# Kernel tuning notes

Measured on AMD Instinct MI355X. Metric: run time of the kernel, lower is better.

The kernel has to match this reference:

```python
import jax, jax.numpy as jnp
import numpy as np

B, S, D, H = 2, 2048, 2048, 16
HD = D // H          # 128
HALF = HD // 2       # 64
EPS = 1e-6


def setup_inputs() -> dict:
    key = jax.random.key(0)
    ks = jax.random.split(key, 10)
    x = jax.random.normal(ks[0], (B, S, D), jnp.float32)
    # RoPE frequencies: standard theta=10000, per (position, half head dim)
    inv_freq = 1.0 / (10000.0 ** (np.arange(HALF, dtype=np.float64) / HALF))
    ang = np.outer(np.arange(S, dtype=np.float64), inv_freq)  # (S, HALF)
    freqs_cos = jnp.asarray(np.cos(ang), jnp.float32)[:, None, :]  # (S,1,HALF)
    freqs_sin = jnp.asarray(np.sin(ang), jnp.float32)[:, None, :]
    sc = 0.02
    qw = jax.random.normal(ks[1], (D, D), jnp.float32) * sc
    kw = jax.random.normal(ks[2], (D, D), jnp.float32) * sc
    vw = jax.random.normal(ks[3], (D, D), jnp.float32) * sc
    ow = jax.random.normal(ks[4], (D, D), jnp.float32) * sc
    qb = jax.random.normal(ks[5], (D,), jnp.float32) * sc
    kb = jax.random.normal(ks[6], (D,), jnp.float32) * sc
    vb = jax.random.normal(ks[7], (D,), jnp.float32) * sc
    ob = jax.random.normal(ks[8], (D,), jnp.float32) * sc
    qnorm_w = jnp.ones((D,), jnp.float32)
    knorm_w = jnp.ones((D,), jnp.float32)
    return {"x": x, "freqs_cos": freqs_cos, "freqs_sin": freqs_sin,
            "qw": qw, "qb": qb, "kw": kw, "kb": kb, "vw": vw, "vb": vb,
            "ow": ow, "ob": ob, "qnorm_w": qnorm_w, "knorm_w": knorm_w}


def _rmsnorm(h, w):
    # norm in fp32 over full last dim (dim, not per-head), as in the source
    hf = h.astype(jnp.float32)
    inv = jax.lax.rsqrt(jnp.mean(hf * hf, axis=-1, keepdims=True) + EPS)
    return (hf * inv).astype(h.dtype) * w


def _rope(h, cos, sin):
    # h: (B,S,D) -> complex rotation on interleaved pairs per head
    b, s, _ = h.shape
    hp = h.reshape(b, s, H, HALF, 2)
    x1, x2 = hp[..., 0], hp[..., 1]
    c = cos[None]   # (1,S,1,HALF) broadcasts over batch & heads
    sn = sin[None]
    o1 = x1 * c - x2 * sn
    o2 = x1 * sn + x2 * c
    return jnp.stack([o1, o2], axis=-1).reshape(b, s, H * HD)


def reference(x, freqs_cos, freqs_sin, qw, qb, kw, kb, vw, vb, ow, ob, qnorm_w, knorm_w):
    q = _rope(_rmsnorm(x @ qw.T + qb, qnorm_w), freqs_cos, freqs_sin)
    k = _rope(_rmsnorm(x @ kw.T + kb, knorm_w), freqs_cos, freqs_sin)
    v = x @ vw.T + vb
    b, s, _ = x.shape
    qh = q.reshape(b, s, H, HD)
    kh = k.reshape(b, s, H, HD)
    vh = v.reshape(b, s, H, HD)
    scale = 1.0 / jnp.sqrt(jnp.float32(HD))
    att = jnp.einsum('bqhd,bkhd->bhqk', qh, kh) * scale
    p = jax.nn.softmax(att, axis=-1)
    o = jnp.einsum('bhqk,bkhd->bqhd', p, vh).reshape(b, s, D)
    return o @ ow.T + ob
```

## Files before the change

### kernel.cpp

```cpp
#include <hip/hip_runtime.h>
#include <stdint.h>

#define B_SZ 2
#define S_LEN 2048
#define D_DIM 2048
#define NHEAD 16
#define HD 128
#define HALF 64
#define MROWS (B_SZ * S_LEN)

typedef __attribute__((ext_vector_type(8))) __bf16 bf16x8;
typedef __attribute__((ext_vector_type(8))) unsigned short u16x8;
typedef __attribute__((ext_vector_type(4))) float f32x4;
typedef __attribute__((ext_vector_type(16))) float f32x16;
typedef __attribute__((ext_vector_type(4))) unsigned int u32x4;

__device__ inline unsigned short f2bf(float x) {
  union { float f; uint32_t u; } c; c.f = x;
  uint32_t r = (c.u + 0x7fffu + ((c.u >> 16) & 1u)) >> 16;
  return (unsigned short)r;
}

__device__ inline float bf2f(unsigned short b) {
  union { uint32_t u; float f; } c; c.u = (uint32_t)b << 16;
  return c.f;
}

__device__ inline void gll16(const void* g, void* l) {
  __builtin_amdgcn_global_load_lds(
      (const __attribute__((address_space(1))) void*)g,
      (__attribute__((address_space(3))) void*)l,
      16, 0, 0);
}

__global__ void cast_all(const float* __restrict__ x,
                         const float* __restrict__ qw, const float* __restrict__ kw,
                         const float* __restrict__ vw, const float* __restrict__ ow,
                         unsigned short* __restrict__ xb,
                         unsigned short* __restrict__ qwb, unsigned short* __restrict__ kwb,
                         unsigned short* __restrict__ vwb, unsigned short* __restrict__ owb) {
  const int n_x = (MROWS * D_DIM) / 4;
  const int n_w = (D_DIM * D_DIM) / 4;
  const int total = n_x + 4 * n_w;
  int i = blockIdx.x * blockDim.x + threadIdx.x;
  int stride = gridDim.x * blockDim.x;
  for (; i < total; i += stride) {
    const float* src; unsigned short* dst; int off;
    if (i < n_x) { src = x; dst = xb; off = i; }
    else {
      int j = i - n_x;
      int seg = j >> 20;
      off = j & (n_w - 1);
      src = seg == 0 ? qw : seg == 1 ? kw : seg == 2 ? vw : ow;
      dst = seg == 0 ? qwb : seg == 1 ? kwb : seg == 2 ? vwb : owb;
    }
    float4 v = reinterpret_cast<const float4*>(src)[off];
    ushort4 o;
    o.x = f2bf(v.x); o.y = f2bf(v.y); o.z = f2bf(v.z); o.w = f2bf(v.w);
    reinterpret_cast<ushort4*>(dst)[off] = o;
  }
}

template <int MODE>
__global__ __launch_bounds__(256) void gemm_bt(
    const unsigned short* __restrict__ A, const unsigned short* __restrict__ Bt,
    const float* __restrict__ bias, void* __restrict__ C0,
    unsigned short* __restrict__ C1, unsigned short* __restrict__ C2,
    int M, int N, int K) {
  __shared__ __align__(16) unsigned short As[128 * 32];
  __shared__ __align__(16) unsigned short Bs[128 * 32];
  const int tid = threadIdx.x;
  const int lane = tid & 63;
  const int wave = tid >> 6;
  const int nbn = N >> 7;
  const int xcd = blockIdx.x & 7;
  const int w = blockIdx.x >> 3;
  const int bm = w & 31;
  const int bn = xcd * (nbn >> 3) + (w >> 5);
  const int wr = wave >> 1, wc = wave & 1;
  const int lm = lane & 15, lg = lane >> 4;

  f32x4 acc[4][4] = {};

  for (int k0 = 0; k0 < K; k0 += 32) {
    __syncthreads();
#pragma unroll
    for (int j = 0; j < 2; ++j) {
      int ob = wave * 2048 + j * 1024;
      int o = ob + lane * 16;
      int row = o >> 6;
      int col = (o & 63) >> 1;
      const unsigned short* ga = A + (size_t)(bm * 128 + row) * K + k0 + col;
      gll16(ga, (char*)As + ob);
      const unsigned short* gb = Bt + (size_t)(bn * 128 + row) * K + k0 + col;
      gll16(gb, (char*)Bs + ob);
    }
    __syncthreads();

    bf16x8 af[4], bfr[4];
#pragma unroll
    for (int mi = 0; mi < 4; ++mi)
      af[mi] = *reinterpret_cast<const bf16x8*>(
          &As[(wr * 64 + mi * 16 + lm) * 32 + lg * 8]);
#pragma unroll
    for (int ni = 0; ni < 4; ++ni)
      bfr[ni] = *reinterpret_cast<const bf16x8*>(
          &Bs[(wc * 64 + ni * 16 + lm) * 32 + lg * 8]);
#pragma unroll
    for (int mi = 0; mi < 4; ++mi)
#pragma unroll
      for (int ni = 0; ni < 4; ++ni)
        acc[mi][ni] = __builtin_amdgcn_mfma_f32_16x16x32_bf16(
            af[mi], bfr[ni], acc[mi][ni], 0, 0, 0);
  }

#pragma unroll
  for (int ni = 0; ni < 4; ++ni) {
    int col = bn * 128 + wc * 64 + ni * 16 + lm;
    float bv = bias[col];
    if constexpr (MODE == 3) {
      int seg = col >> 11;
      int c2 = col & (D_DIM - 1);
#pragma unroll
      for (int mi = 0; mi < 4; ++mi) {
        int row0 = bm * 128 + wr * 64 + mi * 16 + lg * 4;
        if (seg == 2) {
          int b = row0 >> 11, s0 = row0 & (S_LEN - 1);
          int h = c2 >> 7, d = c2 & (HD - 1);
          ushort4 o;
          o.x = f2bf(acc[mi][ni][0] + bv);
          o.y = f2bf(acc[mi][ni][1] + bv);
          o.z = f2bf(acc[mi][ni][2] + bv);
          o.w = f2bf(acc[mi][ni][3] + bv);
          size_t oi = ((((size_t)(b * NHEAD + h) * (S_LEN / 64) + (s0 >> 6)) * HD + d) << 6)
                      + (s0 & 63);
          *reinterpret_cast<ushort4*>(C2 + oi) = o;
        } else {
          unsigned short* dst = (seg == 0) ? (unsigned short*)C0 : C1;
#pragma unroll
          for (int r = 0; r < 4; ++r)
            dst[(size_t)(row0 + r) * D_DIM + c2] = f2bf(acc[mi][ni][r] + bv);
        }
      }
    } else {
      float* out = (float*)C0;
#pragma unroll
      for (int mi = 0; mi < 4; ++mi) {
        int row0 = bm * 128 + wr * 64 + mi * 16 + lg * 4;
#pragma unroll
        for (int r = 0; r < 4; ++r)
          out[(size_t)(row0 + r) * N + col] = acc[mi][ni][r] + bv;
      }
    }
  }
}

__global__ __launch_bounds__(256) void norm_rope2(
    const unsigned short* __restrict__ qin, const unsigned short* __restrict__ kin,
    const float* __restrict__ qnw, const float* __restrict__ knw,
    const float* __restrict__ cosb, const float* __restrict__ sinb,
    unsigned short* __restrict__ qout, unsigned short* __restrict__ kout,
    float qscale) {
  const int isK = blockIdx.x >> 12;
  const int row = blockIdx.x & (MROWS - 1);
  const int pos = row & (S_LEN - 1);
  const unsigned short* hr = (isK ? kin : qin) + (size_t)row * D_DIM;
  const float* w = isK ? knw : qnw;
  const float outscale = isK ? 1.0f : qscale;
  const int t = threadIdx.x;
  const int d = t * 8;

  u16x8 hv = *reinterpret_cast<const u16x8*>(hr + d);
  float a[8];
#pragma unroll
  for (int i = 0; i < 8; ++i) a[i] = bf2f(hv[i]);
  float ss = 0.f;
#pragma unroll
  for (int i = 0; i < 8; ++i) ss += a[i] * a[i];
#pragma unroll
  for (int off = 32; off > 0; off >>= 1) ss += __shfl_down(ss, off);
  __shared__ float red[4];
  if ((t & 63) == 0) red[t >> 6] = ss;
  __syncthreads();
  float tot = red[0] + red[1] + red[2] + red[3];
  float inv = rsqrtf(tot * (1.0f / D_DIM) + 1e-6f) * outscale;

  const int p = (d & (HD - 1)) >> 1;
  const float* cp = cosb + pos * HALF + p;
  const float* sp = sinb + pos * HALF + p;
  const float* wp = w + d;

  float c0 = cp[0], c1 = cp[1], c2 = cp[2], c3 = cp[3];
  float s0 = sp[0], s1 = sp[1], s2 = sp[2], s3 = sp[3];
#pragma unroll
  for (int i = 0; i < 8; ++i) a[i] = a[i] * inv * wp[i];
  u16x8 o;
  o[0] = f2bf(a[0] * c0 - a[1] * s0);
  o[1] = f2bf(a[0] * s0 + a[1] * c0);
  o[2] = f2bf(a[2] * c1 - a[3] * s1);
  o[3] = f2bf(a[2] * s1 + a[3] * c1);
  o[4] = f2bf(a[4] * c2 - a[5] * s2);
  o[5] = f2bf(a[4] * s2 + a[5] * c2);
  o[6] = f2bf(a[6] * c3 - a[7] * s3);
  o[7] = f2bf(a[6] * s3 + a[7] * c3);
  if (isK) {
    int hh = t >> 4;
    int dd = d & (HD - 1);
    size_t oi = (((size_t)((row >> 11) * NHEAD + hh) * S_LEN) + pos) * HD + dd;
    *reinterpret_cast<u16x8*>(kout + oi) = o;
  } else {
    *reinterpret_cast<u16x8*>(qout + (size_t)row * D_DIM + d) = o;
  }
}

__global__ __launch_bounds__(512) void attn_kernel(
    const unsigned short* __restrict__ Q, const unsigned short* __restrict__ Kh,
    const unsigned short* __restrict__ Vt, unsigned short* __restrict__ O) {
  const int idx = blockIdx.x;
  const int swz = (idx & 7) * 32 + (idx >> 3);
  const int qb = swz & 7;
  const int h = (swz >> 3) & 15;
  const int b = swz >> 7;

  const int tid = threadIdx.x;
  const int lane = tid & 63;
  const int wave = tid >> 6;
  const int l31 = lane & 31;
  const int hh = lane >> 5;

  const size_t qbase = (size_t)b * S_LEN * D_DIM + (size_t)h * HD;
  const size_t hbase = (size_t)(b * NHEAD + h) * S_LEN * HD;
  const int q0w = qb * 256 + wave * 32;

  __shared__ __align__(16) unsigned short Ks[2 * 128 * 128];
  __shared__ __align__(16) unsigned short Vs[2 * 128 * 64];

  bf16x8 qf[8];
#pragma unroll
  for (int ds_ = 0; ds_ < 8; ++ds_)
    qf[ds_] = *reinterpret_cast<const bf16x8*>(
        Q + qbase + (size_t)(q0w + l31) * D_DIM + ds_ * 16 + hh * 8);

  f32x16 oacc[4] = {};
  float mrow = -1e30f, lrow = 0.f;

  const int pbase = wave * 1024 + (lane << 4);

  auto stageK = [&](int buf, int tix) {
    const unsigned short* ksrc = Kh + hbase + (size_t)tix * (128 * HD);
#pragma unroll
    for (int j = 0; j < 4; ++j) {
      int p = pbase + j * 8192;
      int kr = p >> 8;
      int kc = ((p >> 4) & 15) ^ ((kr & 7) ^ ((kr >> 3) & 7));
      gll16(ksrc + kr * 128 + kc * 8, (char*)Ks + buf * 32768 + p);
    }
  };
  auto stageV = [&](int tix) {
    const unsigned short* vsrc = Vt + hbase + (size_t)tix * (128 * HD);
#pragma unroll
    for (int j = 0; j < 4; ++j) {
      int p = pbase + j * 8192;
      int vr = (p & 16383) >> 7;
      int vc = ((p >> 4) & 7) ^ (((vr & 7) ^ ((vr >> 3) & 7)) & 7);
      gll16(vsrc + (p >> 14) * (64 * HD) + vr * 64 + vc * 8, (char*)Vs + p);
    }
  };

  stageK(0, 0);

  const int NT = S_LEN / 128;
  for (int t = 0; t < NT; ++t) {
    const int cur = t & 1;
    stageV(t);
    stageK(cur ^ 1, (t + 1 < NT) ? t + 1 : t);
    asm volatile("s_waitcnt vmcnt(8)" ::: "memory");
    __builtin_amdgcn_sched_barrier(0);
    __builtin_amdgcn_s_barrier();
    __builtin_amdgcn_sched_barrier(0);

    const char* kbp = (const char*)Ks + cur * 32768;
    f32x16 sc[4] = {};
    __builtin_amdgcn_s_setprio(1);
#pragma unroll
    for (int ds_ = 0; ds_ < 8; ++ds_) {
#pragma unroll
      for (int j = 0; j < 4; ++j) {
        int r = j * 32 + l31;
        bf16x8 kf = *reinterpret_cast<const bf16x8*>(
            kbp + r * 256 + (((ds_ * 2 + hh) ^ ((r & 7) ^ ((r >> 3) & 7))) << 4));
        sc[j] = __builtin_amdgcn_mfma_f32_32x32x16_bf16(kf, qf[ds_], sc[j], 0, 0, 0);
      }
    }
    __builtin_amdgcn_s_setprio(0);

    float m0[16];
#pragma unroll
    for (int r = 0; r < 16; ++r)
      m0[r] = fmaxf(fmaxf(sc[0][r], sc[1][r]), fmaxf(sc[2][r], sc[3][r]));
#pragma unroll
    for (int r = 0; r < 8; ++r) m0[r] = fmaxf(m0[r], m0[r + 8]);
#pragma unroll
    for (int r = 0; r < 4; ++r) m0[r] = fmaxf(m0[r], m0[r + 4]);
    float mx = fmaxf(fmaxf(m0[0], m0[1]), fmaxf(m0[2], m0[3]));
    mx = fmaxf(mx, __shfl_xor(mx, 32));
    if (__any(mx > mrow + 8.0f)) {
      float nm = fmaxf(mrow, mx);
      float alpha = exp2f(mrow - nm);
      mrow = nm;
      lrow *= alpha;
#pragma unroll
      for (int r = 0; r < 16; ++r) {
        int qr = (r & 3) + 8 * (r >> 2) + 4 * hh;
        float av = __shfl(alpha, qr);
        oacc[0][r] *= av; oacc[1][r] *= av; oacc[2][r] *= av; oacc[3][r] *= av;
      }
    }
#pragma unroll
    for (int j = 0; j < 4; ++j)
#pragma unroll
      for (int r = 0; r < 16; ++r) sc[j][r] = exp2f(sc[j][r] - mrow);
    float s0[16];
#pragma unroll
    for (int r = 0; r < 16; ++r)
      s0[r] = (sc[0][r] + sc[1][r]) + (sc[2][r] + sc[3][r]);
#pragma unroll
    for (int r = 0; r < 8; ++r) s0[r] += s0[r + 8];
#pragma unroll
    for (int r = 0; r < 4; ++r) s0[r] += s0[r + 4];
    lrow += (s0[0] + s0[1]) + (s0[2] + s0[3]);

    uint32_t w[32];
#pragma unroll
    for (int X = 0; X < 4; ++X) {
#pragma unroll
      for (int g = 0; g < 4; ++g) {
        uint32_t lo, hi;
        float a0 = sc[X][4 * g], a1 = sc[X][4 * g + 1];
        float a2 = sc[X][4 * g + 2], a3 = sc[X][4 * g + 3];
        asm("v_cvt_pk_bf16_f32 %0, %1, %2" : "=v"(lo) : "v"(a0), "v"(a1));
        asm("v_cvt_pk_bf16_f32 %0, %1, %2" : "=v"(hi) : "v"(a2), "v"(a3));
        w[X * 8 + g * 2] = lo; w[X * 8 + g * 2 + 1] = hi;
      }
    }
    bf16x8 pa[8];
#pragma unroll
    for (int s = 0; s < 8; ++s) {
      int wb = (s >> 1) * 8 + (s & 1) * 4;
      uint32_t le = w[wb], he = w[wb + 1], lo_ = w[wb + 2], ho = w[wb + 3];
      asm("v_permlane32_swap_b32 %0, %1" : "+v"(le), "+v"(lo_));
      asm("v_permlane32_swap_b32 %0, %1" : "+v"(he), "+v"(ho));
      u32x4 fr = {le, he, lo_, ho};
      pa[s] = __builtin_bit_cast(bf16x8, fr);
    }

    asm volatile("s_waitcnt vmcnt(4)" ::: "memory");
    __builtin_amdgcn_sched_barrier(0);
    __builtin_amdgcn_s_barrier();
    __builtin_amdgcn_sched_barrier(0);

    const char* vbp = (const char*)Vs;
    __builtin_amdgcn_s_setprio(1);
#pragma unroll
    for (int db = 0; db < 4; ++db) {
      int d = db * 32 + l31;
      int fv = ((d & 7) ^ ((d >> 3) & 7)) & 7;
#pragma unroll
      for (int ks = 0; ks < 8; ++ks) {
        bf16x8 vv = *reinterpret_cast<const bf16x8*>(
            vbp + (ks >> 2) * 16384 + d * 128 + ((((ks & 3) * 2 + hh) ^ fv) << 4));
        oacc[db] = __builtin_amdgcn_mfma_f32_32x32x16_bf16(pa[ks], vv, oacc[db], 0, 0, 0);
      }
    }
    __builtin_amdgcn_s_setprio(0);

    __builtin_amdgcn_sched_barrier(0);
    __builtin_amdgcn_s_barrier();
    __builtin_amdgcn_sched_barrier(0);
  }

  lrow += __shfl_xor(lrow, 32);
  float inv_[16];
#pragma unroll
  for (int r = 0; r < 16; ++r) {
    int qr = (r & 3) + 8 * (r >> 2) + 4 * hh;
    inv_[r] = 1.0f / __shfl(lrow, qr);
  }
#pragma unroll
  for (int db = 0; db < 4; ++db) {
#pragma unroll
    for (int r = 0; r < 16; ++r) {
      int qr = (r & 3) + 8 * (r >> 2) + 4 * hh;
      O[qbase + (size_t)(q0w + qr) * D_DIM + db * 32 + l31] =
          f2bf(oacc[db][r] * inv_[r]);
    }
  }
}

extern "C" void kernel_launch(void* const* d_in, const int* in_sizes, int n_in,
                              void* d_out, int out_size, void* d_ws, size_t ws_size,
                              hipStream_t stream) {
  const float* x   = (const float*)d_in[0];
  const float* fc  = (const float*)d_in[1];
  const float* fs  = (const float*)d_in[2];
  const float* qw  = (const float*)d_in[3];
  const float* qb  = (const float*)d_in[4];
  const float* kw  = (const float*)d_in[5];
  const float* kb  = (const float*)d_in[6];
  const float* vw  = (const float*)d_in[7];
  const float* vb  = (const float*)d_in[8];
  const float* ow  = (const float*)d_in[9];
  const float* ob  = (const float*)d_in[10];
  const float* qnw = (const float*)d_in[11];
  const float* knw = (const float*)d_in[12];
  float* out = (float*)d_out;

  const size_t MSD = (size_t)MROWS * D_DIM;
  const size_t WSZ = (size_t)D_DIM * D_DIM;
  char* ws = (char*)d_ws;
  unsigned short* xb   = (unsigned short*)ws; ws += MSD * 2;
  unsigned short* qwb  = (unsigned short*)ws; ws += WSZ * 2;
  unsigned short* kwb  = (unsigned short*)ws; ws += WSZ * 2;
  unsigned short* vwb  = (unsigned short*)ws; ws += WSZ * 2;
  unsigned short* owb  = (unsigned short*)ws; ws += WSZ * 2;
  float*          cbias = (float*)ws;         ws += 3 * D_DIM * 4;
  unsigned short* qpre = (unsigned short*)ws; ws += MSD * 2;
  unsigned short* kpre = (unsigned short*)ws; ws += MSD * 2;
  unsigned short* qb16 = (unsigned short*)ws; ws += MSD * 2;
  unsigned short* kb16 = (unsigned short*)ws; ws += MSD * 2;
  unsigned short* vt16 = (unsigned short*)ws; ws += MSD * 2;
  unsigned short* ob16 = (unsigned short*)ws; ws += MSD * 2;

  cast_all<<<2048, 256, 0, stream>>>(x, qw, kw, vw, ow, xb, qwb, kwb, vwb, owb);
  hipMemcpyAsync(cbias,              qb, D_DIM * sizeof(float), hipMemcpyDeviceToDevice, stream);
  hipMemcpyAsync(cbias + D_DIM,      kb, D_DIM * sizeof(float), hipMemcpyDeviceToDevice, stream);
  hipMemcpyAsync(cbias + 2 * D_DIM,  vb, D_DIM * sizeof(float), hipMemcpyDeviceToDevice, stream);

  gemm_bt<3><<<dim3((MROWS / 128) * (3 * D_DIM / 128)), 256, 0, stream>>>(
      xb, qwb, cbias, qpre, kpre, vt16, MROWS, 3 * D_DIM, D_DIM);

  const float qscale = 0.08838834764831845f * 1.4426950408889634f;
  norm_rope2<<<2 * MROWS, 256, 0, stream>>>(qpre, kpre, qnw, knw, fc, fs,
                                            qb16, kb16, qscale);

  attn_kernel<<<dim3(S_LEN / 256 * NHEAD * B_SZ), 512, 0, stream>>>(qb16, kb16, vt16, ob16);

  gemm_bt<0><<<dim3((MROWS / 128) * (D_DIM / 128)), 256, 0, stream>>>(
      ob16, owb, ob, out, nullptr, nullptr, MROWS, D_DIM, D_DIM);
}
```

Measured before the change: 323.0 us.

## Double GEMM K-tile to 64 and XOR-swizzle LDS layout

The GEMM main loop now stages 64-wide K slices of A and B into LDS per iteration instead of 32, halving the number of barrier pairs per K sweep. The LDS layout is XOR-swizzled by row so that the 16-byte fragment reads for MFMA avoid bank conflicts, with global loads writing into swizzled positions. This doubles LDS use per block, which may reduce occupancy, and there is still no double buffering.

Result: faster. 291.9 us (median of 2 runs) (-9.6%).

```diff
diff --git a/kernel.cpp b/kernel.cpp
--- a/kernel.cpp
+++ b/kernel.cpp
@@ -67,8 +67,8 @@
     const float* __restrict__ bias, void* __restrict__ C0,
     unsigned short* __restrict__ C1, unsigned short* __restrict__ C2,
     int M, int N, int K) {
-  __shared__ __align__(16) unsigned short As[128 * 32];
-  __shared__ __align__(16) unsigned short Bs[128 * 32];
+  __shared__ __align__(16) unsigned short As[128 * 64];
+  __shared__ __align__(16) unsigned short Bs[128 * 64];
   const int tid = threadIdx.x;
   const int lane = tid & 63;
   const int wave = tid >> 6;
@@ -82,36 +82,41 @@
 
   f32x4 acc[4][4] = {};
 
-  for (int k0 = 0; k0 < K; k0 += 32) {
+  for (int k0 = 0; k0 < K; k0 += 64) {
     __syncthreads();
 #pragma unroll
-    for (int j = 0; j < 2; ++j) {
-      int ob = wave * 2048 + j * 1024;
-      int o = ob + lane * 16;
-      int row = o >> 6;
-      int col = (o & 63) >> 1;
-      const unsigned short* ga = A + (size_t)(bm * 128 + row) * K + k0 + col;
-      gll16(ga, (char*)As + ob);
-      const unsigned short* gb = Bt + (size_t)(bn * 128 + row) * K + k0 + col;
-      gll16(gb, (char*)Bs + ob);
+    for (int r = 0; r < 4; ++r) {
+      int p = r * 4096 + tid * 16;
+      int row = p >> 7;
+      int ch = (p >> 4) & 7;
+      int sc = (ch ^ (row & 7)) << 3;
+      gll16(A + (size_t)(bm * 128 + row) * K + k0 + sc, (char*)As + p);
+      gll16(Bt + (size_t)(bn * 128 + row) * K + k0 + sc, (char*)Bs + p);
     }
     __syncthreads();
 
-    bf16x8 af[4], bfr[4];
-#pragma unroll
-    for (int mi = 0; mi < 4; ++mi)
-      af[mi] = *reinterpret_cast<const bf16x8*>(
-          &As[(wr * 64 + mi * 16 + lm) * 32 + lg * 8]);
-#pragma unroll
-    for (int ni = 0; ni < 4; ++ni)
-      bfr[ni] = *reinterpret_cast<const bf16x8*>(
-          &Bs[(wc * 64 + ni * 16 + lm) * 32 + lg * 8]);
-#pragma unroll
-    for (int mi = 0; mi < 4; ++mi)
-#pragma unroll
-      for (int ni = 0; ni < 4; ++ni)
-        acc[mi][ni] = __builtin_amdgcn_mfma_f32_16x16x32_bf16(
-            af[mi], bfr[ni], acc[mi][ni], 0, 0, 0);
+#pragma unroll
+    for (int kk = 0; kk < 2; ++kk) {
+      bf16x8 af[4], bfr[4];
+#pragma unroll
+      for (int mi = 0; mi < 4; ++mi) {
+        int row = wr * 64 + mi * 16 + lm;
+        af[mi] = *reinterpret_cast<const bf16x8*>(
+            (const char*)As + row * 128 + ((((kk << 2) + lg) ^ (row & 7)) << 4));
+      }
+#pragma unroll
+      for (int ni = 0; ni < 4; ++ni) {
+        int row = wc * 64 + ni * 16 + lm;
+        bfr[ni] = *reinterpret_cast<const bf16x8*>(
+            (const char*)Bs + row * 128 + ((((kk << 2) + lg) ^ (row & 7)) << 4));
+      }
+#pragma unroll
+      for (int mi = 0; mi < 4; ++mi)
+#pragma unroll
+        for (int ni = 0; ni < 4; ++ni)
+          acc[mi][ni] = __builtin_amdgcn_mfma_f32_16x16x32_bf16(
+              af[mi], bfr[ni], acc[mi][ni], 0, 0, 0);
+    }
   }
 
 #pragma unroll
```
